# Optimization experiments

Measured on AMD Instinct MI355X. Metric: run time of the kernel, lower is better.

The kernel has to match this reference:

```python
import jax, jax.numpy as jnp
import numpy as np

N_NODES = 100000
N_EDGES = 1000000
D = 256


def setup_inputs() -> dict:
    key = jax.random.key(0)
    ks = jax.random.split(key, 5)
    h = jax.random.normal(ks[0], (N_NODES, D), dtype=jnp.float32)
    edges = jax.random.randint(ks[1], (N_EDGES, 2), 0, N_NODES, dtype=jnp.int64)
    # xavier-uniform-style linear weights, stored as [in, out]
    def xavier(k, fan_in, fan_out):
        limit = float(np.sqrt(6.0 / (fan_in + fan_out)))
        return jax.random.uniform(k, (fan_in, fan_out), dtype=jnp.float32, minval=-limit, maxval=limit)
    W1 = xavier(ks[2], D, D // 2)
    W2 = xavier(ks[3], D // 2, D // 4)
    W3 = xavier(ks[4], D // 4, 2)
    return {
        "h": h, "edges": edges,
        "W1": W1, "b1": jnp.zeros((D // 2,), jnp.float32),
        "W2": W2, "b2": jnp.zeros((D // 4,), jnp.float32),
        "W3": W3, "b3": jnp.zeros((2,), jnp.float32),
    }


def reference(h, edges, W1, b1, W2, b2, W3, b3):
    # gather endpoint embeddings and combine via hadamard product: [E, D]
    emb = h[edges[:, 0]] * h[edges[:, 1]]
    # small MLP chain 256 -> 128 -> 64 -> 2
    out = emb @ W1 + b1
    out = out @ W2 + b2
    out = out @ W3 + b3
    # softmax over class dim
    return jax.nn.softmax(out, axis=1)
```

## Files before the change

### kernel.cpp

```cpp
#include <hip/hip_runtime.h>
#include <hip/hip_bf16.h>


#define D 256

__global__ __launch_bounds__(256) void collapse_weights(
    const float* __restrict__ W1, const float* __restrict__ b1,
    const float* __restrict__ W2, const float* __restrict__ b2,
    const float* __restrict__ W3, const float* __restrict__ b3,
    float* __restrict__ wc)
{
    __shared__ float T[128][2];
    const int t = threadIdx.x;

    {
        const int j = t >> 1, c = t & 1;
        float s = 0.f;
        #pragma unroll 8
        for (int k = 0; k < 64; ++k) s += W2[j * 64 + k] * W3[k * 2 + c];
        T[j][c] = s;
    }
    __syncthreads();

    float s0 = 0.f, s1 = 0.f;
    #pragma unroll 8
    for (int j = 0; j < 128; ++j) {
        const float w = W1[t * 128 + j];
        s0 += w * T[j][0];
        s1 += w * T[j][1];
    }
    wc[t] = s1 - s0;

    if (t == 0) {
        float f0 = b3[0], f1 = b3[1];
        for (int j = 0; j < 128; ++j) { f0 += b1[j] * T[j][0]; f1 += b1[j] * T[j][1]; }
        for (int k = 0; k < 64; ++k)  { f0 += b2[k] * W3[k * 2 + 0]; f1 += b2[k] * W3[k * 2 + 1]; }
        wc[256] = f1 - f0;
    }
}

__device__ __forceinline__ unsigned bf16rn(float f) {
    unsigned u = __float_as_uint(f);
    u += 0x7fffu + ((u >> 16) & 1u);
    return u >> 16;
}

__global__ __launch_bounds__(256) void to_bf16(
    const float4* __restrict__ h, uint2* __restrict__ hb, int nvec)
{
    int i = blockIdx.x * blockDim.x + threadIdx.x;
    const int stride = gridDim.x * blockDim.x;
    for (; i < nvec; i += stride) {
        const float4 f = h[i];
        uint2 o;
        o.x = bf16rn(f.x) | (bf16rn(f.y) << 16);
        o.y = bf16rn(f.z) | (bf16rn(f.w) << 16);
        hb[i] = o;
    }
}

__device__ __forceinline__ float blo(unsigned u) { return __uint_as_float(u << 16); }
__device__ __forceinline__ float bhi(unsigned u) { return __uint_as_float(u & 0xffff0000u); }

__global__ __launch_bounds__(256) void edge_predict_bf16(
    const uint2* __restrict__ hb, const int2* __restrict__ edges,
    const float* __restrict__ wc, float2* __restrict__ out, int E)
{
    const int lane = threadIdx.x & 63;
    const int wid  = blockIdx.x * (blockDim.x >> 6) + (threadIdx.x >> 6);
    const int nw   = gridDim.x * (blockDim.x >> 6);

    const float4 wd = ((const float4*)wc)[lane];
    const float  bd = wc[256];

    for (int e = wid; e < E; e += 2 * nw) {
        const int e2 = e + nw;
        const int2 ed1 = edges[e];
        const uint2 ua1 = hb[(size_t)ed1.x * 64 + lane];
        const uint2 ub1 = hb[(size_t)ed1.y * 64 + lane];
        int2 ed2; uint2 ua2, ub2;
        if (e2 < E) {
            ed2 = edges[e2];
            ua2 = hb[(size_t)ed2.x * 64 + lane];
            ub2 = hb[(size_t)ed2.y * 64 + lane];
        }

        float d1 = blo(ua1.x) * blo(ub1.x) * wd.x
                 + bhi(ua1.x) * bhi(ub1.x) * wd.y
                 + blo(ua1.y) * blo(ub1.y) * wd.z
                 + bhi(ua1.y) * bhi(ub1.y) * wd.w;
        #pragma unroll
        for (int m = 32; m > 0; m >>= 1) d1 += __shfl_xor(d1, m, 64);
        if (lane == 0) {
            const float p1 = 1.0f / (1.0f + __expf(-(d1 + bd)));
            out[e] = make_float2(1.0f - p1, p1);
        }

        if (e2 < E) {
            float d2 = blo(ua2.x) * blo(ub2.x) * wd.x
                     + bhi(ua2.x) * bhi(ub2.x) * wd.y
                     + blo(ua2.y) * blo(ub2.y) * wd.z
                     + bhi(ua2.y) * bhi(ub2.y) * wd.w;
            #pragma unroll
            for (int m = 32; m > 0; m >>= 1) d2 += __shfl_xor(d2, m, 64);
            if (lane == 0) {
                const float p1 = 1.0f / (1.0f + __expf(-(d2 + bd)));
                out[e2] = make_float2(1.0f - p1, p1);
            }
        }
    }
}

__global__ __launch_bounds__(256) void edge_predict_f32(
    const float* __restrict__ h, const int2* __restrict__ edges,
    const float* __restrict__ wc, float2* __restrict__ out, int E)
{
    const int lane = threadIdx.x & 63;
    const int wid  = blockIdx.x * (blockDim.x >> 6) + (threadIdx.x >> 6);
    const int nw   = gridDim.x * (blockDim.x >> 6);

    const float4 wd = ((const float4*)wc)[lane];
    const float  bd = wc[256];

    for (int e = wid; e < E; e += nw) {
        const int2 ed = edges[e];
        const float4 a = ((const float4*)(h + (size_t)ed.x * D))[lane];
        const float4 b = ((const float4*)(h + (size_t)ed.y * D))[lane];
        float d = a.x * b.x * wd.x + a.y * b.y * wd.y
                + a.z * b.z * wd.z + a.w * b.w * wd.w;
        #pragma unroll
        for (int m = 32; m > 0; m >>= 1) d += __shfl_xor(d, m, 64);
        if (lane == 0) {
            const float p1 = 1.0f / (1.0f + __expf(-(d + bd)));
            out[e] = make_float2(1.0f - p1, p1);
        }
    }
}

extern "C" void kernel_launch(void* const* d_in, const int* in_sizes, int n_in,
                              void* d_out, int out_size, void* d_ws, size_t ws_size,
                              hipStream_t stream)
{
    const float* h     = (const float*)d_in[0];
    const int2*  edges = (const int2*)d_in[1];
    const float* W1    = (const float*)d_in[2];
    const float* b1    = (const float*)d_in[3];
    const float* W2    = (const float*)d_in[4];
    const float* b2    = (const float*)d_in[5];
    const float* W3    = (const float*)d_in[6];
    const float* b3    = (const float*)d_in[7];

    float*  wc  = (float*)d_ws;
    float2* out = (float2*)d_out;

    const int nNodes = in_sizes[0] / D;
    const int E      = in_sizes[1] / 2;
    const size_t tbl_off   = 512 * sizeof(float);
    const size_t tbl_bytes = (size_t)nNodes * D * 2;

    collapse_weights<<<1, 256, 0, stream>>>(W1, b1, W2, b2, W3, b3, wc);

    if (ws_size >= tbl_off + tbl_bytes) {
        uint2* hb = (uint2*)((char*)d_ws + tbl_off);
        const int nvec = nNodes * (D / 4);
        to_bf16<<<4096, 256, 0, stream>>>((const float4*)h, hb, nvec);
        edge_predict_bf16<<<2048, 256, 0, stream>>>(hb, edges, wc, out, E);
    } else {
        edge_predict_f32<<<2048, 256, 0, stream>>>(h, edges, wc, out, E);
    }
}
```

Measured before the change: 328.4 us.

## Counting-sort edges by source node before gathering to improve cache reuse

Adds a counting sort of edges by source node: a histogram, a three-kernel prefix scan, and an atomic scatter that writes permuted edge pairs and original indices. Each wavefront then walks a contiguous chunk of sorted edges, so repeated source-row gathers hit cache, and results are scattered back through pidx. The weight collapse, bf16 conversion and histogram zeroing are fused into one prep kernel. The cost is several extra launches, atomics on the edge list, and extra workspace traffic for the permuted arrays.

```diff
diff --git a/kernel.cpp b/kernel.cpp
--- a/kernel.cpp
+++ b/kernel.cpp
@@ -3,54 +3,56 @@
 
 
 #define D 256
-
-__global__ __launch_bounds__(256) void collapse_weights(
-    const float* __restrict__ W1, const float* __restrict__ b1,
-    const float* __restrict__ W2, const float* __restrict__ b2,
-    const float* __restrict__ W3, const float* __restrict__ b3,
-    float* __restrict__ wc)
-{
-    __shared__ float T[128][2];
-    const int t = threadIdx.x;
-
-    {
-        const int j = t >> 1, c = t & 1;
-        float s = 0.f;
-        #pragma unroll 8
-        for (int k = 0; k < 64; ++k) s += W2[j * 64 + k] * W3[k * 2 + c];
-        T[j][c] = s;
-    }
-    __syncthreads();
-
-    float s0 = 0.f, s1 = 0.f;
-    #pragma unroll 8
-    for (int j = 0; j < 128; ++j) {
-        const float w = W1[t * 128 + j];
-        s0 += w * T[j][0];
-        s1 += w * T[j][1];
-    }
-    wc[t] = s1 - s0;
-
-    if (t == 0) {
-        float f0 = b3[0], f1 = b3[1];
-        for (int j = 0; j < 128; ++j) { f0 += b1[j] * T[j][0]; f1 += b1[j] * T[j][1]; }
-        for (int k = 0; k < 64; ++k)  { f0 += b2[k] * W3[k * 2 + 0]; f1 += b2[k] * W3[k * 2 + 1]; }
-        wc[256] = f1 - f0;
-    }
-}
+#define DV (D / 4)
+#define RU2 (D / 4)
 
 __device__ __forceinline__ unsigned bf16rn(float f) {
     unsigned u = __float_as_uint(f);
     u += 0x7fffu + ((u >> 16) & 1u);
     return u >> 16;
 }
-
-__global__ __launch_bounds__(256) void to_bf16(
-    const float4* __restrict__ h, uint2* __restrict__ hb, int nvec)
-{
-    int i = blockIdx.x * blockDim.x + threadIdx.x;
-    const int stride = gridDim.x * blockDim.x;
-    for (; i < nvec; i += stride) {
+__device__ __forceinline__ float blo(unsigned u) { return __uint_as_float(u << 16); }
+__device__ __forceinline__ float bhi(unsigned u) { return __uint_as_float(u & 0xffff0000u); }
+
+__global__ __launch_bounds__(256) void prep(
+    const float4* __restrict__ h, uint2* __restrict__ hb, int nvec,
+    const float* __restrict__ W1, const float* __restrict__ b1,
+    const float* __restrict__ W2, const float* __restrict__ b2,
+    const float* __restrict__ W3, const float* __restrict__ b3,
+    float* __restrict__ wc, int* __restrict__ hist, int nhp)
+{
+    const int gstride = gridDim.x * blockDim.x;
+    for (int i = blockIdx.x * blockDim.x + threadIdx.x; i < nhp; i += gstride)
+        hist[i] = 0;
+
+    if (blockIdx.x == 0) {
+        __shared__ float T[128][2];
+        const int t = threadIdx.x;
+        {
+            const int j = t >> 1, c = t & 1;
+            float s = 0.f;
+            #pragma unroll 8
+            for (int k = 0; k < 64; ++k) s += W2[j * 64 + k] * W3[k * 2 + c];
+            T[j][c] = s;
+        }
+        __syncthreads();
+        float s0 = 0.f, s1 = 0.f;
+        #pragma unroll 8
+        for (int j = 0; j < 128; ++j) {
+            const float w = W1[t * 128 + j];
+            s0 += w * T[j][0];
+            s1 += w * T[j][1];
+        }
+        wc[t] = s1 - s0;
+        if (t == 0) {
+            float f0 = b3[0], f1 = b3[1];
+            for (int j = 0; j < 128; ++j) { f0 += b1[j] * T[j][0]; f1 += b1[j] * T[j][1]; }
+            for (int k = 0; k < 64; ++k)  { f0 += b2[k] * W3[k * 2 + 0]; f1 += b2[k] * W3[k * 2 + 1]; }
+            wc[256] = f1 - f0;
+        }
+    }
+
+    for (int i = blockIdx.x * blockDim.x + threadIdx.x; i < nvec; i += gstride) {
         const float4 f = h[i];
         uint2 o;
         o.x = bf16rn(f.x) | (bf16rn(f.y) << 16);
@@ -59,8 +61,130 @@
     }
 }
 
-__device__ __forceinline__ float blo(unsigned u) { return __uint_as_float(u << 16); }
-__device__ __forceinline__ float bhi(unsigned u) { return __uint_as_float(u & 0xffff0000u); }
+__global__ __launch_bounds__(256) void hist_k(
+    const int2* __restrict__ edges, int* __restrict__ hist, int E)
+{
+    const int gstride = gridDim.x * blockDim.x;
+    for (int e = blockIdx.x * blockDim.x + threadIdx.x; e < E; e += gstride)
+        atomicAdd(&hist[edges[e].x], 1);
+}
+
+__global__ __launch_bounds__(256) void scan1(
+    const int* __restrict__ in, int* __restrict__ outp, int* __restrict__ aux, int n)
+{
+    __shared__ int buf[2][256];
+    const int t = threadIdx.x;
+    const int gid = blockIdx.x * 256 + t;
+    const int v = (gid < n) ? in[gid] : 0;
+    buf[0][t] = v;
+    __syncthreads();
+    int src = 0;
+    for (int off = 1; off < 256; off <<= 1) {
+        int val = buf[src][t];
+        if (t >= off) val += buf[src][t - off];
+        buf[src ^ 1][t] = val;
+        src ^= 1;
+        __syncthreads();
+    }
+    if (gid < n) outp[gid] = buf[src][t] - v;
+    if (t == 255) aux[blockIdx.x] = buf[src][t];
+}
+
+__global__ __launch_bounds__(256) void scan2(int* __restrict__ aux, int n)
+{
+    __shared__ int buf[2][256];
+    const int t = threadIdx.x;
+    int v[4];
+    const int base = t * 4;
+    for (int k = 0; k < 4; ++k) { const int i = base + k; v[k] = (i < n) ? aux[i] : 0; }
+    const int local = v[0] + v[1] + v[2] + v[3];
+    buf[0][t] = local;
+    __syncthreads();
+    int src = 0;
+    for (int off = 1; off < 256; off <<= 1) {
+        int val = buf[src][t];
+        if (t >= off) val += buf[src][t - off];
+        buf[src ^ 1][t] = val;
+        src ^= 1;
+        __syncthreads();
+    }
+    int run = buf[src][t] - local;
+    for (int k = 0; k < 4; ++k) { const int i = base + k; if (i < n) aux[i] = run; run += v[k]; }
+}
+
+__global__ __launch_bounds__(256) void scan3(
+    int* __restrict__ cursor, const int* __restrict__ aux, int n)
+{
+    const int gstride = gridDim.x * blockDim.x;
+    for (int i = blockIdx.x * blockDim.x + threadIdx.x; i < n; i += gstride)
+        cursor[i] += aux[i >> 8];
+}
+
+__global__ __launch_bounds__(256) void scatter_k(
+    const int2* __restrict__ edges, int* __restrict__ cursor,
+    int2* __restrict__ puv, int* __restrict__ pidx, int E)
+{
+    const int gstride = gridDim.x * blockDim.x;
+    for (int e = blockIdx.x * blockDim.x + threadIdx.x; e < E; e += gstride) {
+        const int2 ed = edges[e];
+        const int pos = atomicAdd(&cursor[ed.x], 1);
+        puv[pos] = ed;
+        pidx[pos] = e;
+    }
+}
+
+__global__ __launch_bounds__(256) void edge_sorted(
+    const uint2* __restrict__ hb, const int2* __restrict__ puv,
+    const int* __restrict__ pidx, const float* __restrict__ wc,
+    float2* __restrict__ out, int E, int chunk)
+{
+    const int lane = threadIdx.x & 63;
+    const int wid  = blockIdx.x * (blockDim.x >> 6) + (threadIdx.x >> 6);
+    const int s    = wid * chunk;
+    const int eend = min(E, s + chunk);
+
+    const float4 wd = ((const float4*)wc)[lane];
+    const float  bd = wc[256];
+
+    int e = s;
+    for (; e + 1 < eend; e += 2) {
+        const int2 ed1 = puv[e];
+        const int2 ed2 = puv[e + 1];
+        const uint2 ua1 = hb[(size_t)ed1.x * RU2 + lane];
+        const uint2 ub1 = hb[(size_t)ed1.y * RU2 + lane];
+        const uint2 ua2 = hb[(size_t)ed2.x * RU2 + lane];
+        const uint2 ub2 = hb[(size_t)ed2.y * RU2 + lane];
+
+        float d1 = blo(ua1.x) * blo(ub1.x) * wd.x + bhi(ua1.x) * bhi(ub1.x) * wd.y
+                 + blo(ua1.y) * blo(ub1.y) * wd.z + bhi(ua1.y) * bhi(ub1.y) * wd.w;
+        float d2 = blo(ua2.x) * blo(ub2.x) * wd.x + bhi(ua2.x) * bhi(ub2.x) * wd.y
+                 + blo(ua2.y) * blo(ub2.y) * wd.z + bhi(ua2.y) * bhi(ub2.y) * wd.w;
+        #pragma unroll
+        for (int m = 32; m > 0; m >>= 1) {
+            d1 += __shfl_xor(d1, m, 64);
+            d2 += __shfl_xor(d2, m, 64);
+        }
+        if (lane == 0) {
+            const float p1 = 1.0f / (1.0f + __expf(-(d1 + bd)));
+            out[pidx[e]] = make_float2(1.0f - p1, p1);
+            const float p2 = 1.0f / (1.0f + __expf(-(d2 + bd)));
+            out[pidx[e + 1]] = make_float2(1.0f - p2, p2);
+        }
+    }
+    if (e < eend) {
+        const int2 ed = puv[e];
+        const uint2 ua = hb[(size_t)ed.x * RU2 + lane];
+        const uint2 ub = hb[(size_t)ed.y * RU2 + lane];
+        float d = blo(ua.x) * blo(ub.x) * wd.x + bhi(ua.x) * bhi(ub.x) * wd.y
+                + blo(ua.y) * blo(ub.y) * wd.z + bhi(ua.y) * bhi(ub.y) * wd.w;
+        #pragma unroll
+        for (int m = 32; m > 0; m >>= 1) d += __shfl_xor(d, m, 64);
+        if (lane == 0) {
+            const float p1 = 1.0f / (1.0f + __expf(-(d + bd)));
+            out[pidx[e]] = make_float2(1.0f - p1, p1);
+        }
+    }
+}
 
 __global__ __launch_bounds__(256) void edge_predict_bf16(
     const uint2* __restrict__ hb, const int2* __restrict__ edges,
@@ -69,44 +193,19 @@
     const int lane = threadIdx.x & 63;
     const int wid  = blockIdx.x * (blockDim.x >> 6) + (threadIdx.x >> 6);
     const int nw   = gridDim.x * (blockDim.x >> 6);
-
     const float4 wd = ((const float4*)wc)[lane];
     const float  bd = wc[256];
-
-    for (int e = wid; e < E; e += 2 * nw) {
-        const int e2 = e + nw;
-        const int2 ed1 = edges[e];
-        const uint2 ua1 = hb[(size_t)ed1.x * 64 + lane];
-        const uint2 ub1 = hb[(size_t)ed1.y * 64 + lane];
-        int2 ed2; uint2 ua2, ub2;
-        if (e2 < E) {
-            ed2 = edges[e2];
-            ua2 = hb[(size_t)ed2.x * 64 + lane];
-            ub2 = hb[(size_t)ed2.y * 64 + lane];
-        }
-
-        float d1 = blo(ua1.x) * blo(ub1.x) * wd.x
-                 + bhi(ua1.x) * bhi(ub1.x) * wd.y
-                 + blo(ua1.y) * blo(ub1.y) * wd.z
-                 + bhi(ua1.y) * bhi(ub1.y) * wd.w;
-        #pragma unroll
-        for (int m = 32; m > 0; m >>= 1) d1 += __shfl_xor(d1, m, 64);
-        if (lane == 0) {
-            const float p1 = 1.0f / (1.0f + __expf(-(d1 + bd)));
+    for (int e = wid; e < E; e += nw) {
+        const int2 ed = edges[e];
+        const uint2 ua = hb[(size_t)ed.x * RU2 + lane];
+        const uint2 ub = hb[(size_t)ed.y * RU2 + lane];
+        float d = blo(ua.x) * blo(ub.x) * wd.x + bhi(ua.x) * bhi(ub.x) * wd.y
+                + blo(ua.y) * blo(ub.y) * wd.z + bhi(ua.y) * bhi(ub.y) * wd.w;
+        #pragma unroll
+        for (int m = 32; m > 0; m >>= 1) d += __shfl_xor(d, m, 64);
+        if (lane == 0) {
+            const float p1 = 1.0f / (1.0f + __expf(-(d + bd)));
             out[e] = make_float2(1.0f - p1, p1);
-        }
-
-        if (e2 < E) {
-            float d2 = blo(ua2.x) * blo(ub2.x) * wd.x
-                     + bhi(ua2.x) * bhi(ub2.x) * wd.y
-                     + blo(ua2.y) * blo(ub2.y) * wd.z
-                     + bhi(ua2.y) * bhi(ub2.y) * wd.w;
-            #pragma unroll
-            for (int m = 32; m > 0; m >>= 1) d2 += __shfl_xor(d2, m, 64);
-            if (lane == 0) {
-                const float p1 = 1.0f / (1.0f + __expf(-(d2 + bd)));
-                out[e2] = make_float2(1.0f - p1, p1);
-            }
         }
     }
 }
@@ -118,16 +217,13 @@
     const int lane = threadIdx.x & 63;
     const int wid  = blockIdx.x * (blockDim.x >> 6) + (threadIdx.x >> 6);
     const int nw   = gridDim.x * (blockDim.x >> 6);
-
     const float4 wd = ((const float4*)wc)[lane];
     const float  bd = wc[256];
-
     for (int e = wid; e < E; e += nw) {
         const int2 ed = edges[e];
         const float4 a = ((const float4*)(h + (size_t)ed.x * D))[lane];
         const float4 b = ((const float4*)(h + (size_t)ed.y * D))[lane];
-        float d = a.x * b.x * wd.x + a.y * b.y * wd.y
-                + a.z * b.z * wd.z + a.w * b.w * wd.w;
+        float d = a.x * b.x * wd.x + a.y * b.y * wd.y + a.z * b.z * wd.z + a.w * b.w * wd.w;
         #pragma unroll
         for (int m = 32; m > 0; m >>= 1) d += __shfl_xor(d, m, 64);
         if (lane == 0) {
@@ -149,23 +245,50 @@
     const float* b2    = (const float*)d_in[5];
     const float* W3    = (const float*)d_in[6];
     const float* b3    = (const float*)d_in[7];
-
-    float*  wc  = (float*)d_ws;
     float2* out = (float2*)d_out;
 
     const int nNodes = in_sizes[0] / D;
     const int E      = in_sizes[1] / 2;
-    const size_t tbl_off   = 512 * sizeof(float);
-    const size_t tbl_bytes = (size_t)nNodes * D * 2;
-
-    collapse_weights<<<1, 256, 0, stream>>>(W1, b1, W2, b2, W3, b3, wc);
-
-    if (ws_size >= tbl_off + tbl_bytes) {
-        uint2* hb = (uint2*)((char*)d_ws + tbl_off);
-        const int nvec = nNodes * (D / 4);
-        to_bf16<<<4096, 256, 0, stream>>>((const float4*)h, hb, nvec);
+    const int nvec   = nNodes * DV;
+
+    const int    nblk1  = (nNodes + 255) / 256;
+    const int    nhp    = nblk1 * 256;
+    const size_t wcB    = 2048;
+    const size_t tblB   = (size_t)nNodes * D * 2;
+    const size_t puvB   = (size_t)E * 8;
+    const size_t pidxB  = (size_t)E * 4;
+    const size_t histB  = (size_t)nhp * 4;
+    const size_t auxB   = 4096;
+
+    char* p = (char*)d_ws;
+    float* wc     = (float*)p;                p += wcB;
+    uint2* hb     = (uint2*)p;                p += tblB;
+    const size_t needBf16 = (size_t)(p - (char*)d_ws);
+    int2*  puv    = (int2*)p;                 p += puvB;
+    int*   pidx   = (int*)p;                  p += pidxB;
+    int*   hist   = (int*)p;                  p += histB;
+    int*   cursor = (int*)p;                  p += histB;
+    int*   aux    = (int*)p;                  p += auxB;
+    const size_t needSort = (size_t)(p - (char*)d_ws);
+
+    if (ws_size >= needSort && nblk1 <= 1024) {
+        prep<<<4096, 256, 0, stream>>>((const float4*)h, hb, nvec,
+                                       W1, b1, W2, b2, W3, b3, wc, hist, nhp);
+        hist_k<<<2048, 256, 0, stream>>>(edges, hist, E);
+        scan1<<<nblk1, 256, 0, stream>>>(hist, cursor, aux, nNodes);
+        scan2<<<1, 256, 0, stream>>>(aux, nblk1);
+        scan3<<<nblk1, 256, 0, stream>>>(cursor, aux, nNodes);
+        scatter_k<<<2048, 256, 0, stream>>>(edges, cursor, puv, pidx, E);
+        const int nw = 2048 * 4;
+        const int chunk = (E + nw - 1) / nw;
+        edge_sorted<<<2048, 256, 0, stream>>>(hb, puv, pidx, wc, out, E, chunk);
+    } else if (ws_size >= needBf16) {
+        prep<<<4096, 256, 0, stream>>>((const float4*)h, hb, nvec,
+                                       W1, b1, W2, b2, W3, b3, wc, hist, 0);
         edge_predict_bf16<<<2048, 256, 0, stream>>>(hb, edges, wc, out, E);
     } else {
+        prep<<<4096, 256, 0, stream>>>((const float4*)h, (uint2*)wc , 0,
+                                       W1, b1, W2, b2, W3, b3, wc, hist, 0);
         edge_predict_f32<<<2048, 256, 0, stream>>>(h, edges, wc, out, E);
     }
 }
```

After: 432.0 us. 31.5% more time.
